# Kernel optimization log

Hardware: AMD Instinct MI355X
Metric: run time of the kernel (lower is better)

## Reference

```python
import jax, jax.numpy as jnp
import numpy as np

ALPHA = 0.2   # LeakyReLU negative slope (init arg alpha)
H = 256       # hidden_dim
U = 1024      # user pairs -> 2U user nodes
M = 64        # UAV nodes
D = 2 * U     # uniform out-degree per UAV (edges sorted by source)
N = 2 * U + M
E = M * D


def _lstm_dir(x, w_ih, w_hh, b):
    # x: [T, B, I] -> outputs [T, B, Hc]; b = b_ih + b_hh (they only ever add)
    Hc = w_hh.shape[1]
    B = x.shape[1]
    def step(carry, xt):
        h, c = carry
        g = xt @ w_ih.T + h @ w_hh.T + b          # [B, 4*Hc], gate order i,f,g,o
        i, f, gg, o = jnp.split(g, 4, axis=-1)
        c = jax.nn.sigmoid(f) * c + jax.nn.sigmoid(i) * jnp.tanh(gg)
        h = jax.nn.sigmoid(o) * jnp.tanh(c)
        return (h, c), h
    h0 = jnp.zeros((B, Hc), x.dtype)
    _, hs = jax.lax.scan(step, (h0, h0), x)
    return hs


def _bilstm(x, wih, whh, b):
    # wih: [2, 4Hc, I]; whh: [2, 4Hc, Hc]; b: [2, 4Hc]; dir 0 = fwd, 1 = reverse
    fwd = _lstm_dir(x, wih[0], whh[0], b[0])
    rev = _lstm_dir(x[::-1], wih[1], whh[1], b[1])[::-1]
    return jnp.concatenate([fwd, rev], axis=-1)   # [T, B, 2*Hc]


def _mlp2(h, w1, b1, w2, b2):
    h = jax.nn.relu(h @ w1.T + b1)
    return jax.nn.relu(h @ w2.T + b2)


def _forward(x, edge_index, users_num,
             ul_wih, ul_whh, ul_b, uav_lin_w, uav_lin_b,
             msg_w1, msg_b1, msg_w2, msg_b2,
             wq_w, wq_b, wr_w, wr_b, att_w, att_b,
             upd_w1, upd_b1, upd_w2, upd_b2,
             uavl_wih, uavl_whh, uavl_b, lin2_w, lin2_b):
    Un = users_num
    n = x.shape[0]
    m = n - 2 * Un
    # ---- users bidirectional LSTM over the pair (seq_len=2, batch=U) ----
    seq = jnp.stack([x[:Un], x[Un:2 * Un]], axis=0)        # [2, U, 2]
    users = _bilstm(seq, ul_wih, ul_whh, ul_b)             # [2, U, H]
    users = jnp.concatenate([users[0], users[1]], axis=0)  # [2U, H]
    uavs = x[2 * Un:] @ uav_lin_w.T + uav_lin_b            # [M, H]
    h = jnp.concatenate([users, uavs], axis=0)             # [N, H]
    # ---- message passing (flow target_to_source: i=src, aggregate at src) ----
    src, tgt = edge_index[0], edge_index[1]
    xi = h[src]                                            # [E, H]
    xj = h[tgt]                                            # [E, H]
    msg = _mlp2(jnp.concatenate([xi, xj], axis=1), msg_w1, msg_b1, msg_w2, msg_b2)  # [E, H]
    q = xi @ wq_w.T + wq_b
    r = msg @ wr_w.T + wr_b
    a = jax.nn.leaky_relu(jnp.concatenate([q, r], axis=1) @ att_w.T + att_b, ALPHA)  # [E,1]
    # segment softmax: edges sorted by source, uniform degree -> reshape [M, D]
    a = jax.nn.softmax(a.reshape(m, -1), axis=1).reshape(-1, 1)
    # ---- scatter-mean aggregate over source index ----
    agg = jax.ops.segment_sum(a * msg, src, num_segments=n)          # [N, H]
    cnt = jax.ops.segment_sum(jnp.ones((src.shape[0],), x.dtype), src, num_segments=n)
    agg = agg / jnp.maximum(cnt, 1.0)[:, None]
    # ---- update ----
    h2 = _mlp2(jnp.concatenate([agg, h], axis=1), upd_w1, upd_b1, upd_w2, upd_b2)  # [N, H]
    uav_seq = h2[2 * Un:][:, None, :]                      # [M, 1, H]
    uav_out = _bilstm(uav_seq, uavl_wih, uavl_whh, uavl_b)[:, 0, :]  # [M, H]
    out = jnp.concatenate([h2[:2 * Un], uav_out], axis=0)
    return jax.nn.sigmoid(out @ lin2_w.T + lin2_b)         # [N, 2]


def setup_inputs():
    key = jax.random.key(0)
    ks = iter(jax.random.split(key, 32))
    p = lambda *s: jax.random.normal(next(ks), s, jnp.float32) * 0.05
    Hc = H // 2
    x = jax.random.uniform(next(ks), (N, 2), jnp.float32)
    src = jnp.repeat(2 * U + jnp.arange(M), D)
    tgt = jnp.tile(jnp.arange(2 * U), M)
    edge_index = jnp.stack([src, tgt]).astype(jnp.int32)
    return dict(
        x=x, edge_index=edge_index, users_num=U,
        ul_wih=p(2, 4 * Hc, 2), ul_whh=p(2, 4 * Hc, Hc), ul_b=p(2, 4 * Hc),
        uav_lin_w=p(H, 2), uav_lin_b=p(H),
        msg_w1=p(H, 2 * H), msg_b1=p(H), msg_w2=p(H, H), msg_b2=p(H),
        wq_w=p(H, H), wq_b=p(H), wr_w=p(H, H), wr_b=p(H),
        att_w=p(1, 2 * H), att_b=p(1),
        upd_w1=p(H, 2 * H), upd_b1=p(H), upd_w2=p(H, H), upd_b2=p(H),
        uavl_wih=p(2, 4 * Hc, H), uavl_whh=p(2, 4 * Hc, Hc), uavl_b=p(2, 4 * Hc),
        lin2_w=p(2, H), lin2_b=p(2),
    )


def reference(x, edge_index, users_num,
              ul_wih, ul_whh, ul_b, uav_lin_w, uav_lin_b,
              msg_w1, msg_b1, msg_w2, msg_b2,
              wq_w, wq_b, wr_w, wr_b, att_w, att_b,
              upd_w1, upd_b1, upd_w2, upd_b2,
              uavl_wih, uavl_whh, uavl_b, lin2_w, lin2_b):
    return _forward(x, edge_index, users_num,
                    ul_wih, ul_whh, ul_b, uav_lin_w, uav_lin_b,
                    msg_w1, msg_b1, msg_w2, msg_b2,
                    wq_w, wq_b, wr_w, wr_b, att_w, att_b,
                    upd_w1, upd_b1, upd_w2, upd_b2,
                    uavl_wih, uavl_whh, uavl_b, lin2_w, lin2_b)
```

## Files before the change

kernel.cpp:

```cpp
#include <hip/hip_runtime.h>
#include <hip/hip_bf16.h>
#include <math.h>

#define UQ   1024
#define NUQ  2048
#define MQ   64
#define NN   2112
#define HD   256

typedef __attribute__((ext_vector_type(4))) float f32x4;
typedef __attribute__((ext_vector_type(8))) __bf16 bf16x8;

#define OFF_HB    0u
#define OFF_HUF   65536u
#define OFF_PUBF  1146880u
#define OFF_PB    2195456u
#define OFF_SPR   2260992u
#define OFF_ATT   2261248u
#define OFF_WHHT  2263552u
#define OFF_WIHT  2787840u
#define OFF_W1F   3836416u
#define OFF_W2F   4098560u
#define OFF_UW1F  4229632u
#define OFF_UW2F  4491776u
#define OFF_CREC  4622848u
#define OFF_H2U   5687808u

__device__ __forceinline__ float sigm(float v) { return 1.f / (1.f + expf(-v)); }

__device__ __forceinline__ int huf_idx(int row, int k) {
  return (((row >> 6) * 8 + (k >> 5)) * 4 + ((row >> 4) & 3)) * 512 +
         (((k >> 3) & 3) * 16 + (row & 15)) * 8 + (k & 7);
}
__device__ __forceinline__ int pubf_idx(int row, int k) {
  return (((row >> 8) * 8 + (k >> 5)) * 16 + ((row >> 4) & 15)) * 512 +
         (((k >> 3) & 3) * 16 + (row & 15)) * 8 + (k & 7);
}

__device__ __forceinline__ void gl16(const void* g, void* l) {
  __builtin_amdgcn_global_load_lds((const __attribute__((address_space(1))) void*)g,
                                   (__attribute__((address_space(3))) void*)l, 16, 0, 0);
}

__device__ void tile_transpose_perm(const float* __restrict__ in, int in_ld,
                                    float* __restrict__ out, int out_ld,
                                    int k0, int c0) {
  __shared__ float ldt[64][68];
  const int t = threadIdx.x;
  {
    const int ci = t >> 2, kq = t & 3;
    const int c = c0 + ci;
    const int row = (c & 3) * 128 + (c >> 2);
    const float* src = in + row * in_ld + k0 + kq * 16;
#pragma unroll
    for (int e = 0; e < 4; ++e)
      *(f32x4*)&ldt[ci][kq * 16 + e * 4] = *(const f32x4*)(src + e * 4);
  }
  __syncthreads();
  {
    const int kk = t >> 2, cq = t & 3;
    float* dst = out + (k0 + kk) * out_ld + c0 + cq * 16;
#pragma unroll
    for (int e4 = 0; e4 < 4; ++e4) {
      f32x4 v;
#pragma unroll
      for (int j = 0; j < 4; ++j) v[j] = ldt[cq * 16 + e4 * 4 + j][kk];
      *(f32x4*)(dst + e4 * 4) = v;
    }
// ... 54 lines not shown
  } else if (b < 112) {
    frag_cast16<256>(msg_w2, (b - 96) * 16, (__bf16*)(ws + OFF_W2F));
  } else if (b < 128) {
    frag_cast16<512>(msg_w1, (b - 112) * 16, (__bf16*)(ws + OFF_W1F));
  } else if (b < 144) {
    frag_cast16<512>(upd_w1, (b - 128) * 16, (__bf16*)(ws + OFF_UW1F));
  } else if (b < 160) {
    frag_cast16<256>(upd_w2, (b - 144) * 16, (__bf16*)(ws + OFF_UW2F));
  } else {
    float* wqa = (float*)(ws + OFF_ATT);
    float* vv  = wqa + 256;
    float* c0  = wqa + 512;
    float sa = 0.f, sr = 0.f;
    for (int j = 0; j < 256; ++j) {
      sa += att_w[j]       * wq_w[j * 256 + t];
      sr += att_w[256 + j] * wr_w[j * 256 + t];
    }
    wqa[t] = sa; vv[t] = sr;
    __shared__ float red[256];
    red[t] = att_w[t] * wq_b[t] + att_w[256 + t] * wr_b[t];
    __syncthreads();
    for (int s = 128; s > 0; s >>= 1) { if (t < s) red[t] += red[t + s]; __syncthreads(); }
    if (t == 0) c0[0] = red[0] + att_b[0];
  }
}

__global__ __launch_bounds__(256) void k1_embed(
    const float* __restrict__ x, const float* __restrict__ ul_wih,
    const float* __restrict__ ul_b, const float* __restrict__ uav_lin_w,
    const float* __restrict__ uav_lin_b, char* __restrict__ ws)
{
  __bf16* huf = (__bf16*)(ws + OFF_HUF);
  const int b = blockIdx.x, tid = threadIdx.x;
  if (b < 256) {
    const float* whhT = (const float*)(ws + OFF_WHHT);
    const int dir = tid >> 7, hc = tid & 127;
    const int u0 = b * 4;
    float wx[4], wy[4], bb[4];
#pragma unroll
    for (int g = 0; g < 4; ++g) {
      int row = g * 128 + hc;
      wx[g] = ul_wih[dir * 1024 + row * 2 + 0];
      wy[g] = ul_wih[dir * 1024 + row * 2 + 1];
      bb[g] = ul_b[dir * 512 + row];
    }
    __shared__ float h1s[2][128][4];
    __shared__ float hout[8][260];
    float c1[4], h1v[4], in1x[4], in1y[4];
#pragma unroll
    for (int uu = 0; uu < 4; ++uu) {
      int u = u0 + uu;
      float ax = x[u * 2], ay = x[u * 2 + 1];
      float bx = x[(UQ + u) * 2], by = x[(UQ + u) * 2 + 1];
      float i0x = dir ? bx : ax, i0y = dir ? by : ay;
      in1x[uu] = dir ? ax : bx; in1y[uu] = dir ? ay : by;
      float gv[4];
#pragma unroll
      for (int g = 0; g < 4; ++g) gv[g] = wx[g] * i0x + wy[g] * i0y + bb[g];
      float ii = sigm(gv[0]), gg = tanhf(gv[2]), oo = sigm(gv[3]);
      c1[uu] = ii * gg;
      h1v[uu] = oo * tanhf(c1[uu]);
      h1s[dir][hc][uu] = h1v[uu];
    }
    __syncthreads();
    float acc[4][4];
#pragma unroll
    for (int uu = 0; uu < 4; ++uu)
#pragma unroll
      for (int g = 0; g < 4; ++g) acc[uu][g] = wx[g] * in1x[uu] + wy[g] * in1y[uu] + bb[g];
#pragma unroll 4
    for (int k = 0; k < 128; ++k) {
      f32x4 hv  = *(const f32x4*)&h1s[dir][k][0];
      f32x4 wv4 = *(const f32x4*)(whhT + dir * 65536 + k * 512 + hc * 4);
#pragma unroll
      for (int uu = 0; uu < 4; ++uu)
#pragma unroll
        for (int g = 0; g < 4; ++g) acc[uu][g] += hv[uu] * wv4[g];
    }
    const int col = dir * 128 + hc;
#pragma unroll
    for (int uu = 0; uu < 4; ++uu) {
      float ii = sigm(acc[uu][0]), ff = sigm(acc[uu][1]);
      float gg = tanhf(acc[uu][2]), oo = sigm(acc[uu][3]);
      float c2 = ff * c1[uu] + ii * gg;
      float h2v = oo * tanhf(c2);
      float va = dir ? h2v : h1v[uu];
      float vb = dir ? h1v[uu] : h2v;
      hout[uu][col] = va;
      hout[4 + uu][col] = vb;
    }
    __syncthreads();
    {
      const int lr = tid >> 5, c = tid & 31;
      bf16x8 v;
#pragma unroll
      for (int e = 0; e < 8; ++e) v[e] = (__bf16)hout[lr][c * 8 + e];
      const int node = (lr < 4) ? (u0 + lr) : (UQ + u0 + lr - 4);
      *(bf16x8*)(huf + huf_idx(node, c * 8)) = v;
    }
  } else {
    float* hb = (float*)(ws + OFF_HB);
    const int j = tid;
    const int mb = (b - 256) * 16;
    for (int m = mb; m < mb + 16; ++m) {
      float xa = x[(NUQ + m) * 2], xb = x[(NUQ + m) * 2 + 1];
      float val = xa * uav_lin_w[j * 2] + xb * uav_lin_w[j * 2 + 1] + uav_lin_b[j];
      hb[m * 256 + j] = val;
      huf[huf_idx(NUQ + m, j)] = (__bf16)val;
    }
  }
}

template<int G, int NKS>
__device__ __forceinline__ void frag_gemm_acc_g(const __bf16* __restrict__ Abase, int g0,
                                                const __bf16* __restrict__ Bbase,
                                                f32x4 acc[G][4]) {
  const int lane = threadIdx.x & 63;
  const int cg = threadIdx.x >> 6;
  for (int ks = 0; ks < NKS; ++ks) {
    bf16x8 Af[G], Bf[4];
#pragma unroll
    for (int g = 0; g < G; ++g)
      Af[g] = *(const bf16x8*)(Abase + ((ks * 4 + g0 + g) * 64 + lane) * 8);
#pragma unroll
    for (int f = 0; f < 4; ++f)
      Bf[f] = *(const bf16x8*)(Bbase + ((ks * 16 + cg * 4 + f) * 64 + lane) * 8);
#pragma unroll
    for (int g = 0; g < G; ++g)
#pragma unroll
      for (int f = 0; f < 4; ++f)
        acc[g][f] = __builtin_amdgcn_mfma_f32_16x16x32_bf16(Af[g], Bf[f], acc[g][f], 0, 0, 0);
  }
}

__global__ __launch_bounds__(256) void k2_proj(const float* __restrict__ msg_b1,
                                               char* __restrict__ ws)
// ... 27 lines not shown
      bf16x8 v;
#pragma unroll
      for (int j = 0; j < 8; ++j) v[j] = (__bf16)ldt[row][ks * 32 + kg * 8 + j];
      const int dst = ((c2 * 8 + ks) * 16 + (r16base + r16l)) * 512 + (kg * 16 + row15) * 8;
      *(bf16x8*)(pubf + dst) = v;
    }
  } else if (b == 64) {
    f32x4 acc[4][4] = {};
    frag_gemm_acc_g<4, 8>(huf + 32 * 16384, 0, w1f, acc);
    float* pb = (float*)(ws + OFF_PB);
#pragma unroll
    for (int g = 0; g < 4; ++g)
#pragma unroll
      for (int f = 0; f < 4; ++f)
#pragma unroll
        for (int r = 0; r < 4; ++r) {
          int row = g * 16 + g16 * 4 + r;
          int col = cg * 64 + f * 16 + cl;
          pb[row * 256 + col] = acc[g][f][r] + msg_b1[col];
        }
  } else {
    const float* hb  = (const float*)(ws + OFF_HB);
    const float* wqa = (const float*)(ws + OFF_ATT);
    const float* c0  = wqa + 512;
    float* spr = (float*)(ws + OFF_SPR);
    if (tid < 64) {
      float s = 0.f;
      for (int k = 0; k < 256; ++k) s += hb[tid * 256 + k] * wqa[k];
      spr[tid] = s + c0[0];
    }
  }
}

__global__ __launch_bounds__(512, 4) void k3_edge(const float* __restrict__ msg_b2,
                                                  char* __restrict__ ws)
{
  const char*  PUBF = (const char*)(ws + OFF_PUBF);
  const float* PB   = (const float*)(ws + OFF_PB);
  const float* spr  = (const float*)(ws + OFF_SPR);
  const float* vv   = (const float*)(ws + OFF_ATT) + 256;
  const char*  W2F  = (const char*)(ws + OFF_W2F);
  float* crec = (float*)(ws + OFF_CREC);

  __shared__ __align__(16) char bufA[2][8192];
  __shared__ __align__(16) char bufB[2][16384];
  __shared__ float plds[8][64];
  __shared__ float redmax[8], wds[8];
  __shared__ float wvs[2][256];

  const int m = blockIdx.x >> 4, ch = blockIdx.x & 15;
  const int tid = threadIdx.x, wave = tid >> 6, lane = tid & 63;
  const int cl = lane & 15, g16 = lane >> 4;
  const int rg = wave >> 2, cg = wave & 3;
  const int rot = (m + ch) & 7;
  const float sm = spr[m];
  const float* pbm = PB + m * 256;
  const char* Abase = PUBF + (ch >> 1) * 131072 + (ch & 1) * 16384;
  const int pbq = ((tid >> 4) & 3) * 8;

  {
    bf16x8 raw = *(const bf16x8*)(Abase + rot * 32768 + tid * 16);
    gl16(W2F + rot * 16384 + tid * 16, &bufB[0][tid * 16]);
    gl16(W2F + rot * 16384 + 8192 + tid * 16, &bufB[0][8192 + tid * 16]);
    f32x4 p0 = *(const f32x4*)(pbm + rot * 32 + pbq);
    f32x4 p1 = *(const f32x4*)(pbm + rot * 32 + pbq + 4);
    bf16x8 a;
#pragma unroll
    for (int r = 0; r < 4; ++r) {
      a[r]     = (__bf16)fmaxf((float)raw[r]     + p0[r], 0.f);
      a[4 + r] = (__bf16)fmaxf((float)raw[4 + r] + p1[r], 0.f);
    }
    *(bf16x8*)(&bufA[0][tid * 16]) = a;
  }
  __syncthreads();

  f32x4 acc[4][4] = {};
  for (int i = 0; i < 8; ++i) {
    const int cur = i & 1;
    bf16x8 arn{};
    f32x4 pn0{}, pn1{};
    if (i < 7) {
      const int ksn = (i + 1 + rot) & 7;
      arn = *(const bf16x8*)(Abase + ksn * 32768 + tid * 16);
      gl16(W2F + ksn * 16384 + tid * 16, &bufB[cur ^ 1][tid * 16]);
      gl16(W2F + ksn * 16384 + 8192 + tid * 16, &bufB[cur ^ 1][8192 + tid * 16]);
      pn0 = *(const f32x4*)(pbm + ksn * 32 + pbq);
      pn1 = *(const f32x4*)(pbm + ksn * 32 + pbq + 4);
    }
    bf16x8 Af[4], Bf[4];
#pragma unroll
    for (int g = 0; g < 4; ++g)
      Af[g] = *(const bf16x8*)(&bufA[cur][((rg * 4 + g) * 64 + lane) * 16]);
#pragma unroll
    for (int f = 0; f < 4; ++f)
      Bf[f] = *(const bf16x8*)(&bufB[cur][((cg * 4 + f) * 64 + lane) * 16]);
    __builtin_amdgcn_s_setprio(1);
#pragma unroll
    for (int g = 0; g < 4; ++g)
#pragma unroll
      for (int f = 0; f < 4; ++f)
        acc[g][f] = __builtin_amdgcn_mfma_f32_16x16x32_bf16(Af[g], Bf[f], acc[g][f], 0, 0, 0);
    __builtin_amdgcn_s_setprio(0);
    if (i < 7) {
      bf16x8 a;
#pragma unroll
      for (int r = 0; r < 4; ++r) {
        a[r]     = (__bf16)fmaxf((float)arn[r]     + pn0[r], 0.f);
        a[4 + r] = (__bf16)fmaxf((float)arn[4 + r] + pn1[r], 0.f);
      }
      *(bf16x8*)(&bufA[cur ^ 1][tid * 16]) = a;
    }
    __syncthreads();
  }

  float p[4][4] = {};
#pragma unroll
  for (int f = 0; f < 4; ++f) {
    const int j = cg * 64 + f * 16 + cl;
    const float b2j = msg_b2[j], vj = vv[j];
#pragma unroll
    for (int g = 0; g < 4; ++g)
#pragma unroll
      for (int r = 0; r < 4; ++r) {
        float mv = fmaxf(acc[g][f][r] + b2j, 0.f);
        acc[g][f][r] = mv;
        p[g][r] += mv * vj;
      }
  }
#pragma unroll
  for (int mask = 1; mask < 16; mask <<= 1)
#pragma unroll
    for (int g = 0; g < 4; ++g)
#pragma unroll
      for (int r = 0; r < 4; ++r) p[g][r] += __shfl_xor(p[g][r], mask);
  if (cl == 0) {
#pragma unroll
    for (int g = 0; g < 4; ++g)
#pragma unroll
      for (int r = 0; r < 4; ++r) plds[wave][g * 16 + g16 * 4 + r] = p[g][r];
  }
  __syncthreads();

  float lr[4][4], wm = -3.4e38f;
#pragma unroll
  for (int g = 0; g < 4; ++g)
#pragma unroll
    for (int r = 0; r < 4; ++r) {
      int row = g * 16 + g16 * 4 + r;
      float l = plds[rg * 4 + 0][row] + plds[rg * 4 + 1][row] +
                plds[rg * 4 + 2][row] + plds[rg * 4 + 3][row] + sm;
      l = l > 0.f ? l : 0.2f * l;
      lr[g][r] = l;
      wm = fmaxf(wm, l);
    }
  wm = fmaxf(wm, __shfl_xor(wm, 16));
  wm = fmaxf(wm, __shfl_xor(wm, 32));
  if (lane == 0) redmax[wave] = wm;
  __syncthreads();
  float Mc = redmax[0];
#pragma unroll
  for (int i = 1; i < 8; ++i) Mc = fmaxf(Mc, redmax[i]);

  float e[4][4], ds = 0.f;
#pragma unroll
  for (int g = 0; g < 4; ++g)
#pragma unroll
    for (int r = 0; r < 4; ++r) { e[g][r] = __expf(lr[g][r] - Mc); ds += e[g][r]; }
  ds += __shfl_xor(ds, 16);
  ds += __shfl_xor(ds, 32);
  if (lane == 0) wds[wave] = ds;

#pragma unroll
  for (int f = 0; f < 4; ++f) {
    float w = 0.f;
#pragma unroll
    for (int g = 0; g < 4; ++g)
#pragma unroll
      for (int r = 0; r < 4; ++r) w += e[g][r] * acc[g][f][r];
    w += __shfl_xor(w, 16);
    w += __shfl_xor(w, 32);
    if (g16 == 0) wvs[rg][cg * 64 + f * 16 + cl] = w;
  }
  __syncthreads();

  float* rec = crec + (m * 16 + ch) * 260;
  if (tid < 256) rec[tid] = wvs[0][tid] + wvs[1][tid];
  if (tid == 0) rec[256] = Mc;
  if (tid == 1) rec[257] = wds[0] + wds[4];
}

__global__ __launch_bounds__(256) void k56_update(
    const float* __restrict__ upd_b1, const float* __restrict__ upd_b2,
    const float* __restrict__ lin2_w, const float* __restrict__ lin2_b,
    float* __restrict__ out, char* __restrict__ ws)
{
  const __bf16* huf  = (const __bf16*)(ws + OFF_HUF);
  const __bf16* uw1f = (const __bf16*)(ws + OFF_UW1F);
  const __bf16* uw2f = (const __bf16*)(ws + OFF_UW2F);

  __shared__ __align__(16) __bf16 l1f[8 * 2 * 512];
  __shared__ __align__(16) __bf16 aggf[8 * 2 * 512];
  __shared__ float scs[32][16];
  __shared__ float sS[32];
  __shared__ float l2p[4][32][2];

  const int b = blockIdx.x, tid = threadIdx.x;
  const int lane = tid & 63, cg = tid >> 6;
  const int cl = lane & 15, g16 = lane >> 4;

  f32x4 acc[2][4] = {};
  if (b < 64) {
    frag_gemm_acc_g<2, 8>(huf + (b >> 1) * 16384, (b & 1) * 2, uw1f + 8 * 16 * 512, acc);
  } else {
    const int m0 = (b - 64) * 32;
    const float* crec = (const float*)(ws + OFF_CREC);
    if (tid < 32) {
      const int m = m0 + tid;
      float mx = -3.4e38f;
      for (int c = 0; c < 16; ++c) mx = fmaxf(mx, crec[(m * 16 + c) * 260 + 256]);
      float S = 0.f;
      for (int c = 0; c < 16; ++c) {
        float sc = __expf(crec[(m * 16 + c) * 260 + 256] - mx);
        scs[tid][c] = sc;
        S += sc * crec[(m * 16 + c) * 260 + 257];
      }
      sS[tid] = S;
    }
    __syncthreads();
    for (int ml = 0; ml < 32; ++ml) {
      float A = 0.f;
#pragma unroll
      for (int c = 0; c < 16; ++c) A += scs[ml][c] * crec[((m0 + ml) * 16 + c) * 260 + tid];
      float agg = A / sS[ml] * (1.f / 2048.f);
      aggf[((tid >> 5) * 2 + (ml >> 4)) * 512 + (((tid >> 3) & 3) * 16 + (ml & 15)) * 8 + (tid & 7)] =
          (__bf16)agg;
    }
    __syncthreads();
    const int g0 = (b - 64) * 2;
    const __bf16* hufu = huf + 32 * 16384;
    for (int ks = 0; ks < 8; ++ks) {
      bf16x8 Af[2], Bf[4];
#pragma unroll
      for (int g = 0; g < 2; ++g)
        Af[g] = *(const bf16x8*)(aggf + ((ks * 2 + g) * 64 + lane) * 8);
#pragma unroll
      for (int f = 0; f < 4; ++f)
        Bf[f] = *(const bf16x8*)(uw1f + ((ks * 16 + cg * 4 + f) * 64 + lane) * 8);
#pragma unroll
      for (int g = 0; g < 2; ++g)
#pragma unroll
        for (int f = 0; f < 4; ++f)
          acc[g][f] = __builtin_amdgcn_mfma_f32_16x16x32_bf16(Af[g], Bf[f], acc[g][f], 0, 0, 0);
    }
    for (int ks = 8; ks < 16; ++ks) {
      bf16x8 Af[2], Bf[4];
#pragma unroll
      for (int g = 0; g < 2; ++g)
        Af[g] = *(const bf16x8*)(hufu + (((ks - 8) * 4 + g0 + g) * 64 + lane) * 8);
#pragma unroll
      for (int f = 0; f < 4; ++f)
        Bf[f] = *(const bf16x8*)(uw1f + ((ks * 16 + cg * 4 + f) * 64 + lane) * 8);
#pragma unroll
      for (int g = 0; g < 2; ++g)
#pragma unroll
        for (int f = 0; f < 4; ++f)
// ... 156 lines not shown
extern "C" void kernel_launch(void* const* d_in, const int* in_sizes, int n_in,
                              void* d_out, int out_size, void* d_ws, size_t ws_size,
                              hipStream_t stream)
{
  const float* x         = (const float*)d_in[0];
  const float* ul_wih    = (const float*)d_in[3];
  const float* ul_whh    = (const float*)d_in[4];
  const float* ul_b      = (const float*)d_in[5];
  const float* uav_lin_w = (const float*)d_in[6];
  const float* uav_lin_b = (const float*)d_in[7];
  const float* msg_w1    = (const float*)d_in[8];
  const float* msg_b1    = (const float*)d_in[9];
  const float* msg_w2    = (const float*)d_in[10];
  const float* msg_b2    = (const float*)d_in[11];
  const float* wq_w      = (const float*)d_in[12];
  const float* wq_b      = (const float*)d_in[13];
  const float* wr_w      = (const float*)d_in[14];
  const float* wr_b      = (const float*)d_in[15];
  const float* att_w     = (const float*)d_in[16];
  const float* att_b     = (const float*)d_in[17];
  const float* upd_w1    = (const float*)d_in[18];
  const float* upd_b1    = (const float*)d_in[19];
  const float* upd_w2    = (const float*)d_in[20];
  const float* upd_b2    = (const float*)d_in[21];
  const float* uavl_wih  = (const float*)d_in[22];
  const float* uavl_b    = (const float*)d_in[24];
  const float* lin2_w    = (const float*)d_in[25];
  const float* lin2_b    = (const float*)d_in[26];
  char* ws = (char*)d_ws;
  float* out = (float*)d_out;

  k0_prep<<<dim3(161), dim3(256), 0, stream>>>(ul_whh, uavl_wih, msg_w1, msg_w2, upd_w1,
                                               upd_w2, att_w, att_b, wq_w, wq_b, wr_w, wr_b, ws);
  k1_embed<<<dim3(260), dim3(256), 0, stream>>>(x, ul_wih, ul_b, uav_lin_w, uav_lin_b, ws);
  k2_proj<<<dim3(66), dim3(256), 0, stream>>>(msg_b1, ws);
  k3_edge<<<dim3(1024), dim3(512), 0, stream>>>(msg_b2, ws);
  k56_update<<<dim3(66), dim3(256), 0, stream>>>(upd_b1, upd_b2, lin2_w, lin2_b, out, ws);
  k7_final<<<dim3(64), dim3(1024), 0, stream>>>(uavl_b, lin2_w, lin2_b, out, ws);
}
```

Before: 107.5 us.

## Make edge kernel persistent with full W2 resident in LDS and larger chunks

The edge kernel now launches 256 blocks of 1024 threads. Each block loads the whole 128 KB bf16 W2 weight into LDS once, then processes two (UAV, chunk) jobs of 256 edges each, with activations read straight from global memory into registers instead of double-buffered LDS tiles. This removes the repeated W2 staging and the per-k-step barriers, halves the number of softmax partial records that k56 must merge, and has k1 handle 8 users per block. The cost is fewer, larger blocks with heavy LDS use (likely one block per CU), less latency hiding, and a different workspace layout.

```diff
diff --git a/kernel.cpp b/kernel.cpp
--- a/kernel.cpp
+++ b/kernel.cpp
@@ -24,16 +24,12 @@
 #define OFF_UW1F  4229632u
 #define OFF_UW2F  4491776u
 #define OFF_CREC  4622848u
-#define OFF_H2U   5687808u
+#define OFF_H2U   5155328u
 
 __device__ __forceinline__ float sigm(float v) { return 1.f / (1.f + expf(-v)); }
 
 __device__ __forceinline__ int huf_idx(int row, int k) {
   return (((row >> 6) * 8 + (k >> 5)) * 4 + ((row >> 4) & 3)) * 512 +
-         (((k >> 3) & 3) * 16 + (row & 15)) * 8 + (k & 7);
-}
-__device__ __forceinline__ int pubf_idx(int row, int k) {
-  return (((row >> 8) * 8 + (k >> 5)) * 16 + ((row >> 4) & 15)) * 512 +
          (((k >> 3) & 3) * 16 + (row & 15)) * 8 + (k & 7);
 }
 
@@ -154,10 +150,10 @@
 {
   __bf16* huf = (__bf16*)(ws + OFF_HUF);
   const int b = blockIdx.x, tid = threadIdx.x;
-  if (b < 256) {
+  if (b < 128) {
     const float* whhT = (const float*)(ws + OFF_WHHT);
     const int dir = tid >> 7, hc = tid & 127;
-    const int u0 = b * 4;
+    const int u0 = b * 8;
     float wx[4], wy[4], bb[4];
 #pragma unroll
     for (int g = 0; g < 4; ++g) {
@@ -166,42 +162,47 @@
       wy[g] = ul_wih[dir * 1024 + row * 2 + 1];
       bb[g] = ul_b[dir * 512 + row];
     }
-    __shared__ float h1s[2][128][4];
-    __shared__ float hout[8][260];
-    float c1[4], h1v[4], in1x[4], in1y[4];
-#pragma unroll
-    for (int uu = 0; uu < 4; ++uu) {
+    __shared__ float h1s[2][128][8];
+    __shared__ float hout[16][264];
+    float c1[8], h1v[8], in1x[8], in1y[8];
+#pragma unroll
+    for (int uu = 0; uu < 8; ++uu) {
       int u = u0 + uu;
       float ax = x[u * 2], ay = x[u * 2 + 1];
       float bx = x[(UQ + u) * 2], by = x[(UQ + u) * 2 + 1];
       float i0x = dir ? bx : ax, i0y = dir ? by : ay;
       in1x[uu] = dir ? ax : bx; in1y[uu] = dir ? ay : by;
-      float gv[4];
-#pragma unroll
-      for (int g = 0; g < 4; ++g) gv[g] = wx[g] * i0x + wy[g] * i0y + bb[g];
-      float ii = sigm(gv[0]), gg = tanhf(gv[2]), oo = sigm(gv[3]);
+      float gv0 = wx[0] * i0x + wy[0] * i0y + bb[0];
+      float gv2 = wx[2] * i0x + wy[2] * i0y + bb[2];
+      float gv3 = wx[3] * i0x + wy[3] * i0y + bb[3];
+      float ii = sigm(gv0), gg = tanhf(gv2), oo = sigm(gv3);
       c1[uu] = ii * gg;
       h1v[uu] = oo * tanhf(c1[uu]);
       h1s[dir][hc][uu] = h1v[uu];
     }
     __syncthreads();
-    float acc[4][4];
-#pragma unroll
-    for (int uu = 0; uu < 4; ++uu)
+    float acc[8][4];
+#pragma unroll
+    for (int uu = 0; uu < 8; ++uu)
 #pragma unroll
       for (int g = 0; g < 4; ++g) acc[uu][g] = wx[g] * in1x[uu] + wy[g] * in1y[uu] + bb[g];
-#pragma unroll 4
+#pragma unroll 2
     for (int k = 0; k < 128; ++k) {
-      f32x4 hv  = *(const f32x4*)&h1s[dir][k][0];
+      f32x4 hv0 = *(const f32x4*)&h1s[dir][k][0];
+      f32x4 hv1 = *(const f32x4*)&h1s[dir][k][4];
       f32x4 wv4 = *(const f32x4*)(whhT + dir * 65536 + k * 512 + hc * 4);
 #pragma unroll
       for (int uu = 0; uu < 4; ++uu)
 #pragma unroll
-        for (int g = 0; g < 4; ++g) acc[uu][g] += hv[uu] * wv4[g];
+        for (int g = 0; g < 4; ++g) acc[uu][g] += hv0[uu] * wv4[g];
+#pragma unroll
+      for (int uu = 4; uu < 8; ++uu)
+#pragma unroll
+        for (int g = 0; g < 4; ++g) acc[uu][g] += hv1[uu - 4] * wv4[g];
     }
     const int col = dir * 128 + hc;
 #pragma unroll
-    for (int uu = 0; uu < 4; ++uu) {
+    for (int uu = 0; uu < 8; ++uu) {
       float ii = sigm(acc[uu][0]), ff = sigm(acc[uu][1]);
       float gg = tanhf(acc[uu][2]), oo = sigm(acc[uu][3]);
       float c2 = ff * c1[uu] + ii * gg;
@@ -209,21 +210,23 @@
       float va = dir ? h2v : h1v[uu];
       float vb = dir ? h1v[uu] : h2v;
       hout[uu][col] = va;
-      hout[4 + uu][col] = vb;
-    }
-    __syncthreads();
-    {
-      const int lr = tid >> 5, c = tid & 31;
+      hout[8 + uu][col] = vb;
+    }
+    __syncthreads();
+#pragma unroll
+    for (int it = 0; it < 2; ++it) {
+      const int idx = it * 256 + tid;
+      const int lr = idx >> 5, c = idx & 31;
       bf16x8 v;
 #pragma unroll
       for (int e = 0; e < 8; ++e) v[e] = (__bf16)hout[lr][c * 8 + e];
-      const int node = (lr < 4) ? (u0 + lr) : (UQ + u0 + lr - 4);
+      const int node = (lr < 8) ? (u0 + lr) : (UQ + u0 + lr - 8);
       *(bf16x8*)(huf + huf_idx(node, c * 8)) = v;
     }
   } else {
     float* hb = (float*)(ws + OFF_HB);
     const int j = tid;
-    const int mb = (b - 256) * 16;
+    const int mb = (b - 128) * 16;
     for (int m = mb; m < mb + 16; ++m) {
       float xa = x[(NUQ + m) * 2], xb = x[(NUQ + m) * 2 + 1];
       float val = xa * uav_lin_w[j * 2] + xb * uav_lin_w[j * 2 + 1] + uav_lin_b[j];
@@ -317,8 +320,8 @@
   }
 }
 
-__global__ __launch_bounds__(512, 4) void k3_edge(const float* __restrict__ msg_b2,
-                                                  char* __restrict__ ws)
+__global__ __launch_bounds__(1024) void k3_edge(const float* __restrict__ msg_b2,
+                                                char* __restrict__ ws)
 {
   const char*  PUBF = (const char*)(ws + OFF_PUBF);
   const float* PB   = (const float*)(ws + OFF_PB);
@@ -327,151 +330,154 @@
   const char*  W2F  = (const char*)(ws + OFF_W2F);
   float* crec = (float*)(ws + OFF_CREC);
 
-  __shared__ __align__(16) char bufA[2][8192];
-  __shared__ __align__(16) char bufB[2][16384];
-  __shared__ float plds[8][64];
-  __shared__ float redmax[8], wds[8];
-  __shared__ float wvs[2][256];
-
-  const int m = blockIdx.x >> 4, ch = blockIdx.x & 15;
+  __shared__ __align__(16) __bf16 w2l[65536];
+  __shared__ float plds[16][64];
+  __shared__ float redmax[16], wds[16];
+  __shared__ float wvs[4][256];
+
+  const int bid = blockIdx.x;
   const int tid = threadIdx.x, wave = tid >> 6, lane = tid & 63;
   const int cl = lane & 15, g16 = lane >> 4;
   const int rg = wave >> 2, cg = wave & 3;
-  const int rot = (m + ch) & 7;
-  const float sm = spr[m];
-  const float* pbm = PB + m * 256;
-  const char* Abase = PUBF + (ch >> 1) * 131072 + (ch & 1) * 16384;
-  const int pbq = ((tid >> 4) & 3) * 8;
-
-  {
-    bf16x8 raw = *(const bf16x8*)(Abase + rot * 32768 + tid * 16);
-    gl16(W2F + rot * 16384 + tid * 16, &bufB[0][tid * 16]);
-    gl16(W2F + rot * 16384 + 8192 + tid * 16, &bufB[0][8192 + tid * 16]);
-    f32x4 p0 = *(const f32x4*)(pbm + rot * 32 + pbq);
-    f32x4 p1 = *(const f32x4*)(pbm + rot * 32 + pbq + 4);
-    bf16x8 a;
-#pragma unroll
-    for (int r = 0; r < 4; ++r) {
-      a[r]     = (__bf16)fmaxf((float)raw[r]     + p0[r], 0.f);
-      a[4 + r] = (__bf16)fmaxf((float)raw[4 + r] + p1[r], 0.f);
-    }
-    *(bf16x8*)(&bufA[0][tid * 16]) = a;
-  }
+
+#pragma unroll
+  for (int i = 0; i < 8; ++i)
+    gl16(W2F + i * 16384 + tid * 16, (char*)w2l + i * 16384 + tid * 16);
   __syncthreads();
 
-  f32x4 acc[4][4] = {};
-  for (int i = 0; i < 8; ++i) {
-    const int cur = i & 1;
-    bf16x8 arn{};
-    f32x4 pn0{}, pn1{};
-    if (i < 7) {
-      const int ksn = (i + 1 + rot) & 7;
-      arn = *(const bf16x8*)(Abase + ksn * 32768 + tid * 16);
-      gl16(W2F + ksn * 16384 + tid * 16, &bufB[cur ^ 1][tid * 16]);
-      gl16(W2F + ksn * 16384 + 8192 + tid * 16, &bufB[cur ^ 1][8192 + tid * 16]);
-      pn0 = *(const f32x4*)(pbm + ksn * 32 + pbq);
-      pn1 = *(const f32x4*)(pbm + ksn * 32 + pbq + 4);
-    }
-    bf16x8 Af[4], Bf[4];
+  for (int pair = 0; pair < 2; ++pair) {
+    const int job = pair * 256 + bid;
+    const int m = job >> 3, ch = job & 7;
+    const int rot = m & 7;
+    const float sm = spr[m];
+    const char* Abase = PUBF + ch * 131072;
+    const float* pbm = PB + m * 256;
+    const int arow = ((rg * 4) * 64 + lane) * 16;
+
+    bf16x8 raw[4];
+    {
+      const int ks0 = rot;
+#pragma unroll
+      for (int g = 0; g < 4; ++g)
+        raw[g] = *(const bf16x8*)(Abase + ks0 * 16384 + arow + g * 1024);
+    }
+
+    f32x4 acc[4][4] = {};
+    for (int i = 0; i < 8; ++i) {
+      const int ks = (i + rot) & 7;
+      bf16x8 nxt[4];
+      if (i < 7) {
+        const int ksn = (i + 1 + rot) & 7;
+#pragma unroll
+        for (int g = 0; g < 4; ++g)
+          nxt[g] = *(const bf16x8*)(Abase + ksn * 16384 + arow + g * 1024);
+      }
+      f32x4 p0 = *(const f32x4*)(pbm + ks * 32 + g16 * 8);
+      f32x4 p1 = *(const f32x4*)(pbm + ks * 32 + g16 * 8 + 4);
+      bf16x8 Af[4];
+#pragma unroll
+      for (int g = 0; g < 4; ++g) {
+        bf16x8 a;
+#pragma unroll
+        for (int r = 0; r < 4; ++r) {
+          a[r]     = (__bf16)fmaxf((float)raw[g][r]     + p0[r], 0.f);
+          a[4 + r] = (__bf16)fmaxf((float)raw[g][4 + r] + p1[r], 0.f);
+        }
+        Af[g] = a;
+      }
+      bf16x8 Bf[4];
+#pragma unroll
+      for (int f = 0; f < 4; ++f)
+        Bf[f] = *(const bf16x8*)(w2l + ((ks * 16 + cg * 4 + f) * 64 + lane) * 8);
+      __builtin_amdgcn_s_setprio(1);
+#pragma unroll
+      for (int g = 0; g < 4; ++g)
+#pragma unroll
+        for (int f = 0; f < 4; ++f)
+          acc[g][f] = __builtin_amdgcn_mfma_f32_16x16x32_bf16(Af[g], Bf[f], acc[g][f], 0, 0, 0);
+      __builtin_amdgcn_s_setprio(0);
+      if (i < 7) {
+#pragma unroll
+        for (int g = 0; g < 4; ++g) raw[g] = nxt[g];
+      }
+    }
+
+    float p[4][4] = {};
+#pragma unroll
+    for (int f = 0; f < 4; ++f) {
+      const int j = cg * 64 + f * 16 + cl;
+      const float b2j = msg_b2[j], vj = vv[j];
+#pragma unroll
+      for (int g = 0; g < 4; ++g)
+#pragma unroll
+        for (int r = 0; r < 4; ++r) {
+          float mv = fmaxf(acc[g][f][r] + b2j, 0.f);
+          acc[g][f][r] = mv;
+          p[g][r] += mv * vj;
+        }
+    }
+#pragma unroll
+    for (int mask = 1; mask < 16; mask <<= 1)
+#pragma unroll
+      for (int g = 0; g < 4; ++g)
+#pragma unroll
+        for (int r = 0; r < 4; ++r) p[g][r] += __shfl_xor(p[g][r], mask);
+    if (cl == 0) {
+#pragma unroll
+      for (int g = 0; g < 4; ++g)
+#pragma unroll
+        for (int r = 0; r < 4; ++r) plds[wave][g * 16 + g16 * 4 + r] = p[g][r];
+    }
+    __syncthreads();
+
+    float lr[4][4], wm = -3.4e38f;
 #pragma unroll
     for (int g = 0; g < 4; ++g)
-      Af[g] = *(const bf16x8*)(&bufA[cur][((rg * 4 + g) * 64 + lane) * 16]);
-#pragma unroll
-    for (int f = 0; f < 4; ++f)
-      Bf[f] = *(const bf16x8*)(&bufB[cur][((cg * 4 + f) * 64 + lane) * 16]);
-    __builtin_amdgcn_s_setprio(1);
+#pragma unroll
+      for (int r = 0; r < 4; ++r) {
+        int row = g * 16 + g16 * 4 + r;
+        float l = plds[rg * 4 + 0][row] + plds[rg * 4 + 1][row] +
+                  plds[rg * 4 + 2][row] + plds[rg * 4 + 3][row] + sm;
+        l = l > 0.f ? l : 0.2f * l;
+        lr[g][r] = l;
+        wm = fmaxf(wm, l);
+      }
+    wm = fmaxf(wm, __shfl_xor(wm, 16));
+    wm = fmaxf(wm, __shfl_xor(wm, 32));
+    if (lane == 0) redmax[wave] = wm;
+    __syncthreads();
+    float Mc = redmax[0];
+#pragma unroll
+    for (int i = 1; i < 16; ++i) Mc = fmaxf(Mc, redmax[i]);
+
+    float e[4][4], ds = 0.f;
 #pragma unroll
     for (int g = 0; g < 4; ++g)
 #pragma unroll
-      for (int f = 0; f < 4; ++f)
-        acc[g][f] = __builtin_amdgcn_mfma_f32_16x16x32_bf16(Af[g], Bf[f], acc[g][f], 0, 0, 0);
-    __builtin_amdgcn_s_setprio(0);
-    if (i < 7) {
-      bf16x8 a;
-#pragma unroll
-      for (int r = 0; r < 4; ++r) {
-        a[r]     = (__bf16)fmaxf((float)arn[r]     + pn0[r], 0.f);
-        a[4 + r] = (__bf16)fmaxf((float)arn[4 + r] + pn1[r], 0.f);
-      }
-      *(bf16x8*)(&bufA[cur ^ 1][tid * 16]) = a;
-    }
-    __syncthreads();
-  }
-
-  float p[4][4] = {};
-#pragma unroll
-  for (int f = 0; f < 4; ++f) {
-    const int j = cg * 64 + f * 16 + cl;
-    const float b2j = msg_b2[j], vj = vv[j];
-#pragma unroll
-    for (int g = 0; g < 4; ++g)
-#pragma unroll
-      for (int r = 0; r < 4; ++r) {
-        float mv = fmaxf(acc[g][f][r] + b2j, 0.f);
-        acc[g][f][r] = mv;
-        p[g][r] += mv * vj;
-      }
-  }
-#pragma unroll
-  for (int mask = 1; mask < 16; mask <<= 1)
-#pragma unroll
-    for (int g = 0; g < 4; ++g)
-#pragma unroll
-      for (int r = 0; r < 4; ++r) p[g][r] += __shfl_xor(p[g][r], mask);
-  if (cl == 0) {
-#pragma unroll
-    for (int g = 0; g < 4; ++g)
-#pragma unroll
-      for (int r = 0; r < 4; ++r) plds[wave][g * 16 + g16 * 4 + r] = p[g][r];
-  }
-  __syncthreads();
-
-  float lr[4][4], wm = -3.4e38f;
-#pragma unroll
-  for (int g = 0; g < 4; ++g)
-#pragma unroll
-    for (int r = 0; r < 4; ++r) {
-      int row = g * 16 + g16 * 4 + r;
-      float l = plds[rg * 4 + 0][row] + plds[rg * 4 + 1][row] +
-                plds[rg * 4 + 2][row] + plds[rg * 4 + 3][row] + sm;
-      l = l > 0.f ? l : 0.2f * l;
-      lr[g][r] = l;
-      wm = fmaxf(wm, l);
-    }
-  wm = fmaxf(wm, __shfl_xor(wm, 16));
-  wm = fmaxf(wm, __shfl_xor(wm, 32));
-  if (lane == 0) redmax[wave] = wm;
-  __syncthreads();
-  float Mc = redmax[0];
-#pragma unroll
-  for (int i = 1; i < 8; ++i) Mc = fmaxf(Mc, redmax[i]);
-
-  float e[4][4], ds = 0.f;
-#pragma unroll
-  for (int g = 0; g < 4; ++g)
-#pragma unroll
-    for (int r = 0; r < 4; ++r) { e[g][r] = __expf(lr[g][r] - Mc); ds += e[g][r]; }
-  ds += __shfl_xor(ds, 16);
-  ds += __shfl_xor(ds, 32);
-  if (lane == 0) wds[wave] = ds;
-
-#pragma unroll
-  for (int f = 0; f < 4; ++f) {
-    float w = 0.f;
-#pragma unroll
-    for (int g = 0; g < 4; ++g)
-#pragma unroll
-      for (int r = 0; r < 4; ++r) w += e[g][r] * acc[g][f][r];
-    w += __shfl_xor(w, 16);
-    w += __shfl_xor(w, 32);
-    if (g16 == 0) wvs[rg][cg * 64 + f * 16 + cl] = w;
-  }
-  __syncthreads();
-
-  float* rec = crec + (m * 16 + ch) * 260;
-  if (tid < 256) rec[tid] = wvs[0][tid] + wvs[1][tid];
-  if (tid == 0) rec[256] = Mc;
-  if (tid == 1) rec[257] = wds[0] + wds[4];
+      for (int r = 0; r < 4; ++r) { e[g][r] = __expf(lr[g][r] - Mc); ds += e[g][r]; }
+    ds += __shfl_xor(ds, 16);
+    ds += __shfl_xor(ds, 32);
+    if (lane == 0) wds[wave] = ds;
+
+#pragma unroll
+    for (int f = 0; f < 4; ++f) {
+      float w = 0.f;
+#pragma unroll
+      for (int g = 0; g < 4; ++g)
+#pragma unroll
+        for (int r = 0; r < 4; ++r) w += e[g][r] * acc[g][f][r];
+      w += __shfl_xor(w, 16);
+      w += __shfl_xor(w, 32);
+      if (g16 == 0) wvs[rg][cg * 64 + f * 16 + cl] = w;
+    }
+    __syncthreads();
+
+    float* rec = crec + (m * 8 + ch) * 260;
+    if (tid < 256) rec[tid] = wvs[0][tid] + wvs[1][tid] + wvs[2][tid] + wvs[3][tid];
+    if (tid == 0) rec[256] = Mc;
+    if (tid == 1) rec[257] = wds[0] + wds[4] + wds[8] + wds[12];
+    __syncthreads();
+  }
 }
 
 __global__ __launch_bounds__(256) void k56_update(
@@ -485,7 +491,7 @@
 
   __shared__ __align__(16) __bf16 l1f[8 * 2 * 512];
   __shared__ __align__(16) __bf16 aggf[8 * 2 * 512];
-  __shared__ float scs[32][16];
+  __shared__ float scs[32][8];
   __shared__ float sS[32];
   __shared__ float l2p[4][32][2];
 
@@ -502,12 +508,12 @@
     if (tid < 32) {
       const int m = m0 + tid;
       float mx = -3.4e38f;
-      for (int c = 0; c < 16; ++c) mx = fmaxf(mx, crec[(m * 16 + c) * 260 + 256]);
+      for (int c = 0; c < 8; ++c) mx = fmaxf(mx, crec[(m * 8 + c) * 260 + 256]);
       float S = 0.f;
-      for (int c = 0; c < 16; ++c) {
-        float sc = __expf(crec[(m * 16 + c) * 260 + 256] - mx);
+      for (int c = 0; c < 8; ++c) {
+        float sc = __expf(crec[(m * 8 + c) * 260 + 256] - mx);
         scs[tid][c] = sc;
-        S += sc * crec[(m * 16 + c) * 260 + 257];
+        S += sc * crec[(m * 8 + c) * 260 + 257];
       }
       sS[tid] = S;
     }
@@ -515,7 +521,7 @@
     for (int ml = 0; ml < 32; ++ml) {
       float A = 0.f;
 #pragma unroll
-      for (int c = 0; c < 16; ++c) A += scs[ml][c] * crec[((m0 + ml) * 16 + c) * 260 + tid];
+      for (int c = 0; c < 8; ++c) A += scs[ml][c] * crec[((m0 + ml) * 8 + c) * 260 + tid];
       float agg = A / sS[ml] * (1.f / 2048.f);
       aggf[((tid >> 5) * 2 + (ml >> 4)) * 512 + (((tid >> 3) & 3) * 16 + (ml & 15)) * 8 + (tid & 7)] =
           (__bf16)agg;
@@ -738,9 +744,9 @@
 
   k0_prep<<<dim3(161), dim3(256), 0, stream>>>(ul_whh, uavl_wih, msg_w1, msg_w2, upd_w1,
                                                upd_w2, att_w, att_b, wq_w, wq_b, wr_w, wr_b, ws);
-  k1_embed<<<dim3(260), dim3(256), 0, stream>>>(x, ul_wih, ul_b, uav_lin_w, uav_lin_b, ws);
+  k1_embed<<<dim3(132), dim3(256), 0, stream>>>(x, ul_wih, ul_b, uav_lin_w, uav_lin_b, ws);
   k2_proj<<<dim3(66), dim3(256), 0, stream>>>(msg_b1, ws);
-  k3_edge<<<dim3(1024), dim3(512), 0, stream>>>(msg_b2, ws);
+  k3_edge<<<dim3(256), dim3(1024), 0, stream>>>(msg_b2, ws);
   k56_update<<<dim3(66), dim3(256), 0, stream>>>(upd_b1, upd_b2, lin2_w, lin2_b, out, ws);
   k7_final<<<dim3(64), dim3(1024), 0, stream>>>(uavl_b, lin2_w, lin2_b, out, ws);
 }
```

Result: slower. 132.4 us (+23.1%).

## Process two UAVs per edge block sharing user-projection tiles and W2 loads

Applied to the files above, without the earlier changes.

The edge kernel now handles a pair of UAV nodes per block, with 1024 threads covering 256 edges per chunk, so each loaded user-projection tile and W2 fragment feeds two accumulator sets. The grid drops from 1024 to 256 blocks, chunks per UAV go from 16 to 8, and the update kernel's chunk-combining loop is adjusted to match. This cuts redundant global reads of the A and B operands but doubles accumulator registers, runs the softmax epilogue twice in sequence, and leaves fewer blocks to spread across the GPU.

```diff
diff --git a/kernel.cpp b/kernel.cpp
--- a/kernel.cpp
+++ b/kernel.cpp
@@ -24,16 +24,12 @@
 #define OFF_UW1F  4229632u
 #define OFF_UW2F  4491776u
 #define OFF_CREC  4622848u
-#define OFF_H2U   5687808u
+#define OFF_H2U   5155328u
 
 __device__ __forceinline__ float sigm(float v) { return 1.f / (1.f + expf(-v)); }
 
 __device__ __forceinline__ int huf_idx(int row, int k) {
   return (((row >> 6) * 8 + (k >> 5)) * 4 + ((row >> 4) & 3)) * 512 +
-         (((k >> 3) & 3) * 16 + (row & 15)) * 8 + (k & 7);
-}
-__device__ __forceinline__ int pubf_idx(int row, int k) {
-  return (((row >> 8) * 8 + (k >> 5)) * 16 + ((row >> 4) & 15)) * 512 +
          (((k >> 3) & 3) * 16 + (row & 15)) * 8 + (k & 7);
 }
 
@@ -317,8 +313,8 @@
   }
 }
 
-__global__ __launch_bounds__(512, 4) void k3_edge(const float* __restrict__ msg_b2,
-                                                  char* __restrict__ ws)
+__global__ __launch_bounds__(1024) void k3_edge(const float* __restrict__ msg_b2,
+                                                char* __restrict__ ws)
 {
   const char*  PUBF = (const char*)(ws + OFF_PUBF);
   const float* PB   = (const float*)(ws + OFF_PB);
@@ -327,55 +323,61 @@
   const char*  W2F  = (const char*)(ws + OFF_W2F);
   float* crec = (float*)(ws + OFF_CREC);
 
-  __shared__ __align__(16) char bufA[2][8192];
+  __shared__ __align__(16) char bufA0[2][16384];
+  __shared__ __align__(16) char bufA1[2][16384];
   __shared__ __align__(16) char bufB[2][16384];
-  __shared__ float plds[8][64];
-  __shared__ float redmax[8], wds[8];
-  __shared__ float wvs[2][256];
-
-  const int m = blockIdx.x >> 4, ch = blockIdx.x & 15;
+  __shared__ float plds[16][64];
+  __shared__ float redmax[16], wds[16];
+  __shared__ float wvs[4][256];
+
+  const int bid = blockIdx.x;
+  const int ch = bid & 7, mp = bid >> 3;
+  const int m0 = mp * 2, m1 = m0 + 1;
+  const int rot = (mp + ch) & 7;
   const int tid = threadIdx.x, wave = tid >> 6, lane = tid & 63;
   const int cl = lane & 15, g16 = lane >> 4;
   const int rg = wave >> 2, cg = wave & 3;
-  const int rot = (m + ch) & 7;
-  const float sm = spr[m];
-  const float* pbm = PB + m * 256;
-  const char* Abase = PUBF + (ch >> 1) * 131072 + (ch & 1) * 16384;
-  const int pbq = ((tid >> 4) & 3) * 8;
+  const char* Abase = PUBF + ch * 131072;
+  const float* pbm0 = PB + m0 * 256;
+  const float* pbm1 = PB + m1 * 256;
+  const int bq = ((tid >> 4) & 3) * 8;
 
   {
-    bf16x8 raw = *(const bf16x8*)(Abase + rot * 32768 + tid * 16);
+    bf16x8 raw = *(const bf16x8*)(Abase + rot * 16384 + tid * 16);
     gl16(W2F + rot * 16384 + tid * 16, &bufB[0][tid * 16]);
-    gl16(W2F + rot * 16384 + 8192 + tid * 16, &bufB[0][8192 + tid * 16]);
-    f32x4 p0 = *(const f32x4*)(pbm + rot * 32 + pbq);
-    f32x4 p1 = *(const f32x4*)(pbm + rot * 32 + pbq + 4);
-    bf16x8 a;
+    f32x4 q00 = *(const f32x4*)(pbm0 + rot * 32 + bq);
+    f32x4 q01 = *(const f32x4*)(pbm0 + rot * 32 + bq + 4);
+    f32x4 q10 = *(const f32x4*)(pbm1 + rot * 32 + bq);
+    f32x4 q11 = *(const f32x4*)(pbm1 + rot * 32 + bq + 4);
+    bf16x8 a0, a1;
 #pragma unroll
     for (int r = 0; r < 4; ++r) {
-      a[r]     = (__bf16)fmaxf((float)raw[r]     + p0[r], 0.f);
-      a[4 + r] = (__bf16)fmaxf((float)raw[4 + r] + p1[r], 0.f);
-    }
-    *(bf16x8*)(&bufA[0][tid * 16]) = a;
+      float rv = (float)raw[r], rv4 = (float)raw[4 + r];
+      a0[r]     = (__bf16)fmaxf(rv  + q00[r], 0.f);
+      a0[4 + r] = (__bf16)fmaxf(rv4 + q01[r], 0.f);
+      a1[r]     = (__bf16)fmaxf(rv  + q10[r], 0.f);
+      a1[4 + r] = (__bf16)fmaxf(rv4 + q11[r], 0.f);
+    }
+    *(bf16x8*)(&bufA0[0][tid * 16]) = a0;
+    *(bf16x8*)(&bufA1[0][tid * 16]) = a1;
   }
   __syncthreads();
 
-  f32x4 acc[4][4] = {};
+  f32x4 acc0[4][4] = {}, acc1[4][4] = {};
   for (int i = 0; i < 8; ++i) {
     const int cur = i & 1;
-    bf16x8 arn{};
-    f32x4 pn0{}, pn1{};
+    bf16x8 rawn{};
     if (i < 7) {
       const int ksn = (i + 1 + rot) & 7;
-      arn = *(const bf16x8*)(Abase + ksn * 32768 + tid * 16);
+      rawn = *(const bf16x8*)(Abase + ksn * 16384 + tid * 16);
       gl16(W2F + ksn * 16384 + tid * 16, &bufB[cur ^ 1][tid * 16]);
-      gl16(W2F + ksn * 16384 + 8192 + tid * 16, &bufB[cur ^ 1][8192 + tid * 16]);
-      pn0 = *(const f32x4*)(pbm + ksn * 32 + pbq);
-      pn1 = *(const f32x4*)(pbm + ksn * 32 + pbq + 4);
-    }
-    bf16x8 Af[4], Bf[4];
-#pragma unroll
-    for (int g = 0; g < 4; ++g)
-      Af[g] = *(const bf16x8*)(&bufA[cur][((rg * 4 + g) * 64 + lane) * 16]);
+    }
+    bf16x8 Af0[4], Af1[4], Bf[4];
+#pragma unroll
+    for (int g = 0; g < 4; ++g) {
+      Af0[g] = *(const bf16x8*)(&bufA0[cur][((rg * 4 + g) * 64 + lane) * 16]);
+      Af1[g] = *(const bf16x8*)(&bufA1[cur][((rg * 4 + g) * 64 + lane) * 16]);
+    }
 #pragma unroll
     for (int f = 0; f < 4; ++f)
       Bf[f] = *(const bf16x8*)(&bufB[cur][((cg * 4 + f) * 64 + lane) * 16]);
@@ -383,95 +385,111 @@
 #pragma unroll
     for (int g = 0; g < 4; ++g)
 #pragma unroll
-      for (int f = 0; f < 4; ++f)
-        acc[g][f] = __builtin_amdgcn_mfma_f32_16x16x32_bf16(Af[g], Bf[f], acc[g][f], 0, 0, 0);
+      for (int f = 0; f < 4; ++f) {
+        acc0[g][f] = __builtin_amdgcn_mfma_f32_16x16x32_bf16(Af0[g], Bf[f], acc0[g][f], 0, 0, 0);
+        acc1[g][f] = __builtin_amdgcn_mfma_f32_16x16x32_bf16(Af1[g], Bf[f], acc1[g][f], 0, 0, 0);
+      }
     __builtin_amdgcn_s_setprio(0);
     if (i < 7) {
-      bf16x8 a;
+      const int ksn = (i + 1 + rot) & 7;
+      f32x4 q00 = *(const f32x4*)(pbm0 + ksn * 32 + bq);
+      f32x4 q01 = *(const f32x4*)(pbm0 + ksn * 32 + bq + 4);
+      f32x4 q10 = *(const f32x4*)(pbm1 + ksn * 32 + bq);
+      f32x4 q11 = *(const f32x4*)(pbm1 + ksn * 32 + bq + 4);
+      bf16x8 a0, a1;
 #pragma unroll
       for (int r = 0; r < 4; ++r) {
-        a[r]     = (__bf16)fmaxf((float)arn[r]     + pn0[r], 0.f);
-        a[4 + r] = (__bf16)fmaxf((float)arn[4 + r] + pn1[r], 0.f);
+        float rv = (float)rawn[r], rv4 = (float)rawn[4 + r];
+        a0[r]     = (__bf16)fmaxf(rv  + q00[r], 0.f);
+        a0[4 + r] = (__bf16)fmaxf(rv4 + q01[r], 0.f);
+        a1[r]     = (__bf16)fmaxf(rv  + q10[r], 0.f);
+        a1[4 + r] = (__bf16)fmaxf(rv4 + q11[r], 0.f);
       }
-      *(bf16x8*)(&bufA[cur ^ 1][tid * 16]) = a;
-    }
-    __syncthreads();
-  }
-
-  float p[4][4] = {};
-#pragma unroll
-  for (int f = 0; f < 4; ++f) {
-    const int j = cg * 64 + f * 16 + cl;
-    const float b2j = msg_b2[j], vj = vv[j];
+      *(bf16x8*)(&bufA0[cur ^ 1][tid * 16]) = a0;
+      *(bf16x8*)(&bufA1[cur ^ 1][tid * 16]) = a1;
+    }
+    __syncthreads();
+  }
+
+  auto epilogue = [&](f32x4 (&acc)[4][4], float smv, float* rec) {
+    float p[4][4] = {};
+#pragma unroll
+    for (int f = 0; f < 4; ++f) {
+      const int j = cg * 64 + f * 16 + cl;
+      const float b2j = msg_b2[j], vj = vv[j];
+#pragma unroll
+      for (int g = 0; g < 4; ++g)
+#pragma unroll
+        for (int r = 0; r < 4; ++r) {
+          float mv = fmaxf(acc[g][f][r] + b2j, 0.f);
+          acc[g][f][r] = mv;
+          p[g][r] += mv * vj;
+        }
+    }
+#pragma unroll
+    for (int mask = 1; mask < 16; mask <<= 1)
+#pragma unroll
+      for (int g = 0; g < 4; ++g)
+#pragma unroll
+        for (int r = 0; r < 4; ++r) p[g][r] += __shfl_xor(p[g][r], mask);
+    if (cl == 0) {
+#pragma unroll
+      for (int g = 0; g < 4; ++g)
+#pragma unroll
+        for (int r = 0; r < 4; ++r) plds[wave][g * 16 + g16 * 4 + r] = p[g][r];
+    }
+    __syncthreads();
+
+    float lr[4][4], wm = -3.4e38f;
 #pragma unroll
     for (int g = 0; g < 4; ++g)
 #pragma unroll
       for (int r = 0; r < 4; ++r) {
-        float mv = fmaxf(acc[g][f][r] + b2j, 0.f);
-        acc[g][f][r] = mv;
-        p[g][r] += mv * vj;
+        int row = g * 16 + g16 * 4 + r;
+        float l = plds[rg * 4 + 0][row] + plds[rg * 4 + 1][row] +
+                  plds[rg * 4 + 2][row] + plds[rg * 4 + 3][row] + smv;
+        l = l > 0.f ? l : 0.2f * l;
+        lr[g][r] = l;
+        wm = fmaxf(wm, l);
       }
-  }
-#pragma unroll
-  for (int mask = 1; mask < 16; mask <<= 1)
+    wm = fmaxf(wm, __shfl_xor(wm, 16));
+    wm = fmaxf(wm, __shfl_xor(wm, 32));
+    if (lane == 0) redmax[wave] = wm;
+    __syncthreads();
+    float Mc = redmax[0];
+#pragma unroll
+    for (int i = 1; i < 16; ++i) Mc = fmaxf(Mc, redmax[i]);
+
+    float e[4][4], ds = 0.f;
 #pragma unroll
     for (int g = 0; g < 4; ++g)
 #pragma unroll
-      for (int r = 0; r < 4; ++r) p[g][r] += __shfl_xor(p[g][r], mask);
-  if (cl == 0) {
-#pragma unroll
-    for (int g = 0; g < 4; ++g)
-#pragma unroll
-      for (int r = 0; r < 4; ++r) plds[wave][g * 16 + g16 * 4 + r] = p[g][r];
-  }
-  __syncthreads();
-
-  float lr[4][4], wm = -3.4e38f;
-#pragma unroll
-  for (int g = 0; g < 4; ++g)
-#pragma unroll
-    for (int r = 0; r < 4; ++r) {
-      int row = g * 16 + g16 * 4 + r;
-      float l = plds[rg * 4 + 0][row] + plds[rg * 4 + 1][row] +
-                plds[rg * 4 + 2][row] + plds[rg * 4 + 3][row] + sm;
-      l = l > 0.f ? l : 0.2f * l;
-      lr[g][r] = l;
-      wm = fmaxf(wm, l);
-    }
-  wm = fmaxf(wm, __shfl_xor(wm, 16));
-  wm = fmaxf(wm, __shfl_xor(wm, 32));
-  if (lane == 0) redmax[wave] = wm;
-  __syncthreads();
-  float Mc = redmax[0];
-#pragma unroll
-  for (int i = 1; i < 8; ++i) Mc = fmaxf(Mc, redmax[i]);
-
-  float e[4][4], ds = 0.f;
-#pragma unroll
-  for (int g = 0; g < 4; ++g)
-#pragma unroll
-    for (int r = 0; r < 4; ++r) { e[g][r] = __expf(lr[g][r] - Mc); ds += e[g][r]; }
-  ds += __shfl_xor(ds, 16);
-  ds += __shfl_xor(ds, 32);
-  if (lane == 0) wds[wave] = ds;
-
-#pragma unroll
-  for (int f = 0; f < 4; ++f) {
-    float w = 0.f;
-#pragma unroll
-    for (int g = 0; g < 4; ++g)
-#pragma unroll
-      for (int r = 0; r < 4; ++r) w += e[g][r] * acc[g][f][r];
-    w += __shfl_xor(w, 16);
-    w += __shfl_xor(w, 32);
-    if (g16 == 0) wvs[rg][cg * 64 + f * 16 + cl] = w;
-  }
-  __syncthreads();
-
-  float* rec = crec + (m * 16 + ch) * 260;
-  if (tid < 256) rec[tid] = wvs[0][tid] + wvs[1][tid];
-  if (tid == 0) rec[256] = Mc;
-  if (tid == 1) rec[257] = wds[0] + wds[4];
+      for (int r = 0; r < 4; ++r) { e[g][r] = __expf(lr[g][r] - Mc); ds += e[g][r]; }
+    ds += __shfl_xor(ds, 16);
+    ds += __shfl_xor(ds, 32);
+    if (lane == 0) wds[wave] = ds;
+
+#pragma unroll
+    for (int f = 0; f < 4; ++f) {
+      float w = 0.f;
+#pragma unroll
+      for (int g = 0; g < 4; ++g)
+#pragma unroll
+        for (int r = 0; r < 4; ++r) w += e[g][r] * acc[g][f][r];
+      w += __shfl_xor(w, 16);
+      w += __shfl_xor(w, 32);
+      if (g16 == 0) wvs[rg][cg * 64 + f * 16 + cl] = w;
+    }
+    __syncthreads();
+
+    if (tid < 256) rec[tid] = wvs[0][tid] + wvs[1][tid] + wvs[2][tid] + wvs[3][tid];
+    if (tid == 0) rec[256] = Mc;
+    if (tid == 1) rec[257] = wds[0] + wds[4] + wds[8] + wds[12];
+    __syncthreads();
+  };
+
+  epilogue(acc0, spr[m0], crec + (m0 * 8 + ch) * 260);
+  epilogue(acc1, spr[m1], crec + (m1 * 8 + ch) * 260);
 }
 
 __global__ __launch_bounds__(256) void k56_update(
@@ -485,7 +503,7 @@
 
   __shared__ __align__(16) __bf16 l1f[8 * 2 * 512];
   __shared__ __align__(16) __bf16 aggf[8 * 2 * 512];
-  __shared__ float scs[32][16];
+  __shared__ float scs[32][8];
   __shared__ float sS[32];
   __shared__ float l2p[4][32][2];
 
@@ -502,12 +520,12 @@
     if (tid < 32) {
       const int m = m0 + tid;
       float mx = -3.4e38f;
-      for (int c = 0; c < 16; ++c) mx = fmaxf(mx, crec[(m * 16 + c) * 260 + 256]);
+      for (int c = 0; c < 8; ++c) mx = fmaxf(mx, crec[(m * 8 + c) * 260 + 256]);
       float S = 0.f;
-      for (int c = 0; c < 16; ++c) {
-        float sc = __expf(crec[(m * 16 + c) * 260 + 256] - mx);
+      for (int c = 0; c < 8; ++c) {
+        float sc = __expf(crec[(m * 8 + c) * 260 + 256] - mx);
         scs[tid][c] = sc;
-        S += sc * crec[(m * 16 + c) * 260 + 257];
+        S += sc * crec[(m * 8 + c) * 260 + 257];
       }
       sS[tid] = S;
     }
@@ -515,7 +533,7 @@
     for (int ml = 0; ml < 32; ++ml) {
       float A = 0.f;
 #pragma unroll
-      for (int c = 0; c < 16; ++c) A += scs[ml][c] * crec[((m0 + ml) * 16 + c) * 260 + tid];
+      for (int c = 0; c < 8; ++c) A += scs[ml][c] * crec[((m0 + ml) * 8 + c) * 260 + tid];
       float agg = A / sS[ml] * (1.f / 2048.f);
       aggf[((tid >> 5) * 2 + (ml >> 4)) * 512 + (((tid >> 3) & 3) * 16 + (ml & 15)) * 8 + (tid & 7)] =
           (__bf16)agg;
@@ -740,7 +758,7 @@
                                                upd_w2, att_w, att_b, wq_w, wq_b, wr_w, wr_b, ws);
   k1_embed<<<dim3(260), dim3(256), 0, stream>>>(x, ul_wih, ul_b, uav_lin_w, uav_lin_b, ws);
   k2_proj<<<dim3(66), dim3(256), 0, stream>>>(msg_b1, ws);
-  k3_edge<<<dim3(1024), dim3(512), 0, stream>>>(msg_b2, ws);
+  k3_edge<<<dim3(256), dim3(1024), 0, stream>>>(msg_b2, ws);
   k56_update<<<dim3(66), dim3(256), 0, stream>>>(upd_b1, upd_b2, lin2_w, lin2_b, out, ws);
   k7_final<<<dim3(64), dim3(1024), 0, stream>>>(uavl_b, lin2_w, lin2_b, out, ws);
 }
```

New measurement: 272.2 us. +153.3%, slower.
